# Performance work log

Hardware: AMD Instinct MI355X
Metric: run time of the kernel (lower is better)

Reference implementation:

```python
import jax, jax.numpy as jnp
import numpy as np

BATCH, NUM, CONS = 16384, 512, 512


def setup_inputs() -> dict:
    key = jax.random.key(0)
    k1, k2, k3, k4 = jax.random.split(key, 4)
    preds = jax.random.uniform(k1, (BATCH, NUM), dtype=jnp.float32)
    # sparse, mutually-exclusive binary body masks (a literal is pos or neg, not both)
    r = jax.random.randint(k2, (CONS, NUM), 0, 12)
    pos_body = (r == 0).astype(jnp.float32)
    neg_body = (r == 1).astype(jnp.float32)
    head_atom = jax.random.randint(k3, (CONS,), 0, NUM).astype(jnp.int32)
    head_sign = jax.random.randint(k4, (CONS,), 0, 2).astype(jnp.bool_)
    return {"preds": preds, "pos_body": pos_body, "neg_body": neg_body,
            "head_atom": head_atom, "head_sign": head_sign}


def reference(preds, pos_body, neg_body, head_atom, head_sign):
    # apply_iterative with goal=None: Gauss-Seidel sweep over constraints.
    # For constraint c: body value per atom j is pos_body[c,j]*(1-p[:,j]) or
    # neg_body[c,j]*p[:,j]; candidate = 1 - max(0, max_j body value);
    # then head literal is raised (positive) or lowered (negative).
    def step(p, xs):
        pos_row, neg_row, atom, sign = xs
        # [batch, num] elementwise; masks are disjoint so per-atom max == concat-max
        vals = jnp.maximum(pos_row[None, :] * (1.0 - p), neg_row[None, :] * p)
        cand = 1.0 - jnp.maximum(jnp.max(vals, axis=1), 0.0)  # zeros column in torch cat
        prev = jnp.take(p, atom, axis=1)  # [batch]
        upd = jnp.where(sign,
                        jnp.maximum(prev, cand),
                        jnp.minimum(prev, 1.0 - cand))
        p = jax.lax.dynamic_update_slice(p, upd[:, None], (0, atom))
        return p, None

    out, _ = jax.lax.scan(step, preds, (pos_body, neg_body, head_atom, head_sign))
    return out
```

## Files before the change

kernel.cpp:

```cpp
#include <hip/hip_runtime.h>

#define BATCH 16384
#define NUM   512
#define CONS  512
#define ROWS  8
#define ZOFF  (NUM*16)
#define OOFF  (NUM*16 + 16)
#define LDSB  (NUM*16 + 32)
#define NPAD  (CONS + 4)
#define RSTR  84

typedef _Float16 h2 __attribute__((ext_vector_type(2)));
static __device__ __forceinline__ h2 u2h(unsigned u){ return __builtin_bit_cast(h2,u); }
static __device__ __forceinline__ unsigned h2u(h2 h){ return __builtin_bit_cast(unsigned,h); }
static __device__ __forceinline__ h2 hmax2(h2 a,h2 b){ return __builtin_elementwise_max(a,b); }
static __device__ __forceinline__ h2 hmin2(h2 a,h2 b){ return __builtin_elementwise_min(a,b); }
template<int C>
static __device__ __forceinline__ h2 rormax(h2 x) {
  unsigned v = (unsigned)__builtin_amdgcn_mov_dpp((int)h2u(x), C, 0xF, 0xF, true);
  return hmax2(x, u2h(v));
}

__global__ __launch_bounds__(64) void prep_kernel(
    const float* __restrict__ pos, const float* __restrict__ neg,
    const int* __restrict__ head_atom, const int* __restrict__ head_sign,
    unsigned* __restrict__ ents) {
  int c = blockIdx.x, lane = threadIdx.x;
  unsigned* rec = ents + (size_t)c * RSTR;
  if (c >= CONS) {
    for (int t = lane; t < RSTR; t += 64) {
      unsigned v = 0;
      if (t < 32) v = 0x20002000u;
      else if (t < 64) v = 0x20102010u;
      else if (t == 64) v = 0x8000u << 16;
      else if (t < 73) v = ZOFF;
      else if (t < 81) v = OOFF;
      rec[t] = v;
    }
    return;
  }
  __shared__ unsigned short LN[96], LP[96];
  __shared__ unsigned short slotN[64], slotP[64];
  __shared__ unsigned char usedN[64], usedP[64];
  __shared__ unsigned short spill[16][8];
  __shared__ int spn[16];
  __shared__ unsigned short exN[8], exP[8];
  __shared__ int exn, exp_;
  slotN[lane] = ZOFF; slotP[lane] = OOFF;
  usedN[lane] = 0;    usedP[lane] = 0;
  if (lane < 8) { exN[lane] = ZOFF; exP[lane] = OOFF; }
  if (lane < 16) spn[lane] = 0;
  __syncthreads();

  int hp1 = (c >= 1) ? head_atom[c-1] : -1;
  int hp2 = (c >= 2) ? head_atom[c-2] : -1;
  int nN = 0, nP = 0;
  bool fN1=false, fP1=false, fN2=false, fP2=false;
  for (int k = 0; k < NUM/64; ++k) {
    int a = k*64 + lane;
    bool ln = neg[(size_t)c*NUM + a] != 0.f;
    bool lp = pos[(size_t)c*NUM + a] != 0.f;
    bool n1 = ln && (a == hp1), n2 = ln && (a == hp2);
    bool p1 = lp && (a == hp1), p2 = lp && (a == hp2);
    fN1 |= (__ballot(n1) != 0ull); fN2 |= (__ballot(n2) != 0ull);
    fP1 |= (__ballot(p1) != 0ull); fP2 |= (__ballot(p2) != 0ull);
    bool kn = ln && !n1 && !n2;
    bool kp = lp && !p1 && !p2;
    unsigned long long mn = __ballot(kn), mp = __ballot(kp);
    unsigned long long lt = (1ull << lane) - 1ull;
    int rn = nN + (int)__popcll(mn & lt);
    int rp = nP + (int)__popcll(mp & lt);
    if (kn && rn < 96) LN[rn] = (unsigned short)a;
    if (kp && rp < 96) LP[rp] = (unsigned short)a;
    nN += (int)__popcll(mn);
    nP += (int)__popcll(mp);
  }
  __syncthreads();
  if (lane < 16) {
    int r = lane & 7;
    bool isP = lane >= 8;
    const unsigned short* L = isP ? LP : LN;
    int n = isP ? nP : nN; if (n > 96) n = 96;
    unsigned short* slot = isP ? slotP : slotN;
    unsigned char* used = isP ? usedP : usedN;
    int rr = 0;
    for (int t = 0; t < n; ++t) {
      int a = L[t];
      if ((a & 7) == r) {
        if (rr < 8) { int s = rr*8 + r; slot[s] = (unsigned short)(a*16); used[s] = 1; }
        else if (rr < 16) spill[lane][rr-8] = (unsigned short)(a*16);
        ++rr;
      }
    }
    spn[lane] = rr > 8 ? (rr > 16 ? 8 : rr - 8) : 0;
  }
  __syncthreads();
  if (lane < 2) {
    bool isP = lane == 1;
    unsigned short* slot = isP ? slotP : slotN;
    unsigned char* used = isP ? usedP : usedN;
    unsigned short* exb = isP ? exP : exN;
    int base = isP ? 8 : 0;
    int e = 0, scan = 0;
    for (int r = 0; r < 8; ++r) {
      int ns = spn[base + r];
      for (int k = 0; k < ns; ++k) {
        unsigned short v = spill[base + r][k];
        while (scan < 64 && used[scan]) ++scan;
        if (scan < 64) { slot[scan] = v; used[scan] = 1; }
        else if (e < 8) exb[e++] = v;
      }
    }
    if (isP) exp_ = e; else exn = e;
  }
  __syncthreads();

  int hc = head_atom[c];
  unsigned fl = 0;
  if (head_sign[c]) fl |= 1u;
  if (fN1) fl |= 2u;  if (fP1) fl |= 4u;
  if (fN2) fl |= 8u;  if (fP2) fl |= 16u;
  if (hc == hp1) fl |= 32u; else if (hc == hp2) fl |= 64u;
  fl |= ((unsigned)exn << 7) | ((unsigned)exp_ << 11);
  unsigned ho = (unsigned)hc * 16u;
  for (int t = lane; t < RSTR; t += 64) {
    unsigned v;
    if (t < 32) {
      int jp = t >> 4, g = t & 15;
      v = (unsigned)slotN[32*jp + g] | ((unsigned)slotN[32*jp + 16 + g] << 16);
    } else if (t < 64) {
      int tp = t - 32, jp = tp >> 4, g = tp & 15;
      v = (unsigned)slotP[32*jp + g] | ((unsigned)slotP[32*jp + 16 + g] << 16);
    } else if (t == 64) v = ho | (fl << 16);
    else if (t < 73) v = exN[t - 65];
    else if (t < 81) v = exP[t - 73];
    else v = 0;
    rec[t] = v;
  }
}

struct ENT { unsigned w0, w1, w2, w3, mh; };
struct RDv { h2 n0,n1,n2,n3,p0,p1,p2,p3,pv; unsigned mh; };
struct ST  { h2 braw, prevraw; unsigned ho, flu; };

static __device__ __forceinline__ ENT ldent(const unsigned* ents, int c, int g) {
  const unsigned* rec = ents + (size_t)c * RSTR;
  ENT e;
  e.w0 = rec[g]; e.w1 = rec[16+g]; e.w2 = rec[32+g]; e.w3 = rec[48+g];
  e.mh = rec[64];
  return e;
}
static __device__ __forceinline__ void issue_reads(const ENT& E, const char* Pb,
                                                   unsigned pr4, RDv& R) {
  R.n0 = *(const h2*)(Pb + ((E.w0 & 0xFFFFu) + pr4));
  R.n1 = *(const h2*)(Pb + ((E.w0 >> 16)     + pr4));
  R.n2 = *(const h2*)(Pb + ((E.w1 & 0xFFFFu) + pr4));
  R.n3 = *(const h2*)(Pb + ((E.w1 >> 16)     + pr4));
  R.p0 = *(const h2*)(Pb + ((E.w2 & 0xFFFFu) + pr4));
  R.p1 = *(const h2*)(Pb + ((E.w2 >> 16)     + pr4));
  R.p2 = *(const h2*)(Pb + ((E.w3 & 0xFFFFu) + pr4));
  R.p3 = *(const h2*)(Pb + ((E.w3 >> 16)     + pr4));
  R.pv = *(const h2*)(Pb + ((E.mh & 0xFFFFu) + pr4));
  R.mh = E.mh;
}
static __device__ __forceinline__ void combine(const RDv& R, const unsigned* ents,
                                               int c, const char* Pb, unsigned pr4, ST& S) {
  h2 aN = hmax2(hmax2(R.n0, R.n1), hmax2(R.n2, R.n3));
  h2 aP = hmin2(hmin2(R.p0, R.p1), hmin2(R.p2, R.p3));
  unsigned flu = ((unsigned)__builtin_amdgcn_readfirstlane((int)R.mh)) >> 16;
  if (flu & 0x7F80u) {
    const unsigned* rec = ents + (size_t)c * RSTR;
    unsigned xn = (flu >> 7) & 15u, xp = (flu >> 11) & 15u;
    for (unsigned j = 0; j < xn; ++j) aN = hmax2(aN, *(const h2*)(Pb + (rec[65+j] + pr4)));
    for (unsigned j = 0; j < xp; ++j) aP = hmin2(aP, *(const h2*)(Pb + (rec[73+j] + pr4)));
  }
  const h2 one2 = {(_Float16)1.f, (_Float16)1.f};
  h2 bp = hmax2(aN, one2 - aP);
  bp = rormax<0x121>(bp);
  bp = rormax<0x122>(bp);
  bp = rormax<0x124>(bp);
  bp = rormax<0x128>(bp);
  S.braw = bp; S.prevraw = R.pv; S.ho = R.mh & 0xFFFFu; S.flu = flu;
}
static __device__ __forceinline__ h2 finalize(const ST& S, h2 up1, h2 up2,
                                              char* Pb, unsigned pr4, int lane) {
  const h2 one2 = {(_Float16)1.f, (_Float16)1.f};
  unsigned fl = S.flu;
  unsigned mN1 = 0u-((fl>>1)&1u), mP1 = 0u-((fl>>2)&1u);
  unsigned mN2 = 0u-((fl>>3)&1u), mP2 = 0u-((fl>>4)&1u);
  h2 b = S.braw;
  b = hmax2(b, u2h(h2u(up1) & mN1));
  b = hmax2(b, u2h(h2u(one2 - up1) & mP1));
  b = hmax2(b, u2h(h2u(up2) & mN2));
  b = hmax2(b, u2h(h2u(one2 - up2) & mP2));
  unsigned mR1 = 0u-((fl>>5)&1u), mR2 = 0u-((fl>>6)&1u), mRn = ~(mR1|mR2);
  h2 prev = u2h((h2u(up1)&mR1) | (h2u(up2)&mR2) | (h2u(S.prevraw)&mRn));
  unsigned ms = 0u-(fl&1u);
  unsigned hi = h2u(hmax2(prev, one2 - b));
  unsigned lo = h2u(hmin2(prev, b));
  h2 upd = u2h((hi&ms) | (lo&~ms));
  if ((lane & 15) == 0 && !(fl & 0x8000u))
    *(h2*)(Pb + S.ho + pr4) = upd;
  return upd;
}

__global__ __launch_bounds__(64, 2) void solve_kernel(
    const float* __restrict__ preds,
    const unsigned* __restrict__ ents,
    float* __restrict__ out) {
  __shared__ char Pb[LDSB];
  const int lane = threadIdx.x;
  const unsigned pr4 = (unsigned)(lane >> 4) * 4u;
  const int r2 = lane >> 4, cs = lane & 15;
  const size_t row0 = (size_t)blockIdx.x * ROWS;

  if (lane < 4)      *(unsigned*)(Pb + ZOFF + lane*4) = 0u;
  else if (lane < 8) *(unsigned*)(Pb + OOFF + (lane-4)*4) = 0x3C003C00u;

  for (int i = 0; i < 16; ++i) {
    int a = i*32 + cs*2;
    float2 v0 = *(const float2*)(preds + (row0 + 2*r2)     * NUM + a);
    float2 v1 = *(const float2*)(preds + (row0 + 2*r2 + 1) * NUM + a);
    h2 w0 = {(_Float16)v0.x, (_Float16)v1.x};
    h2 w1 = {(_Float16)v0.y, (_Float16)v1.y};
    *(h2*)(Pb + a*16 + r2*4) = w0;
    *(h2*)(Pb + (a+1)*16 + r2*4) = w1;
  }
  __syncthreads();

  const int g = lane & 15;
  ENT E0 = ldent(ents, 0, g), E1 = ldent(ents, 1, g);
  ENT E2 = ldent(ents, 2, g), E3 = ldent(ents, 3, g);
  RDv RA, RB; ST S0, S1;
  issue_reads(E0, Pb, pr4, RA);
  issue_reads(E1, Pb, pr4, RB);
  combine(RA, ents, 0, Pb, pr4, S0);
  h2 up1 = (h2)0.0f, up2 = (h2)0.0f;

  #pragma unroll 1
  for (int i = 0; i < CONS; i += 2) {
    issue_reads(E2, Pb, pr4, RA);
    { h2 u = finalize(S0, up1, up2, Pb, pr4, lane); up2 = up1; up1 = u; }
    combine(RB, ents, i+1, Pb, pr4, S1);
    E2 = ldent(ents, i+4, g);
    issue_reads(E3, Pb, pr4, RB);
    { h2 u = finalize(S1, up1, up2, Pb, pr4, lane); up2 = up1; up1 = u; }
    combine(RA, ents, i+2, Pb, pr4, S0);
    E3 = ldent(ents, i+5, g);
  }

  __syncthreads();
  for (int i = 0; i < 16; ++i) {
    int a = i*32 + cs*2;
    h2 w0 = *(const h2*)(Pb + a*16 + r2*4);
    h2 w1 = *(const h2*)(Pb + (a+1)*16 + r2*4);
    float2 v0 = {(float)w0.x, (float)w1.x};
    float2 v1 = {(float)w0.y, (float)w1.y};
    *(float2*)(out + (row0 + 2*r2)     * NUM + a) = v0;
    *(float2*)(out + (row0 + 2*r2 + 1) * NUM + a) = v1;
  }
}

extern "C" void kernel_launch(void* const* d_in, const int* in_sizes, int n_in,
                              void* d_out, int out_size, void* d_ws, size_t ws_size,
                              hipStream_t stream) {
  (void)in_sizes; (void)n_in; (void)out_size; (void)ws_size;
  const float* preds     = (const float*)d_in[0];
  const float* pos       = (const float*)d_in[1];
  const float* neg       = (const float*)d_in[2];
  const int*   head_atom = (const int*)d_in[3];
  const int*   head_sign = (const int*)d_in[4];

  unsigned* ents = (unsigned*)d_ws;

  prep_kernel<<<NPAD, 64, 0, stream>>>(pos, neg, head_atom, head_sign, ents);
  solve_kernel<<<BATCH / ROWS, 64, 0, stream>>>(preds, ents, (float*)d_out);
}
```

Before: 278.3 us.

## Transpose lane mapping and pack constraint records for vector loads

Lanes now map the row-pair index to lane&3 and the slot group to lane>>2, instead of the reverse. Per-constraint slot words are interleaved so each lane fetches its four offset words with one uint4 load. The cross-lane max reduction is rebuilt to match the new mapping, using two DPP row shifts, a ds_swizzle and a ds_bpermute. Flag handling in finalize switches from mask arithmetic to branches on uniform flags, and the readfirstlane on the flag word is dropped. The swizzle and bpermute go through the LDS crossbar and may add latency on the serial dependency chain, and the coalescing of the preds loads also changes.

```diff
diff --git a/kernel.cpp b/kernel.cpp
--- a/kernel.cpp
+++ b/kernel.cpp
@@ -8,7 +8,7 @@
 #define OOFF  (NUM*16 + 16)
 #define LDSB  (NUM*16 + 32)
 #define NPAD  (CONS + 4)
-#define RSTR  84
+#define RSTR  96
 
 typedef _Float16 h2 __attribute__((ext_vector_type(2)));
 static __device__ __forceinline__ h2 u2h(unsigned u){ return __builtin_bit_cast(h2,u); }
@@ -20,6 +20,14 @@
   unsigned v = (unsigned)__builtin_amdgcn_mov_dpp((int)h2u(x), C, 0xF, 0xF, true);
   return hmax2(x, u2h(v));
 }
+static __device__ __forceinline__ h2 swizmax(h2 x) {
+  unsigned v = (unsigned)__builtin_amdgcn_ds_swizzle((int)h2u(x), 0x401F);
+  return hmax2(x, u2h(v));
+}
+static __device__ __forceinline__ h2 bpermax(h2 x, int bpa) {
+  unsigned v = (unsigned)__builtin_amdgcn_ds_bpermute(bpa, (int)h2u(x));
+  return hmax2(x, u2h(v));
+}
 
 __global__ __launch_bounds__(64) void prep_kernel(
     const float* __restrict__ pos, const float* __restrict__ neg,
@@ -29,12 +37,12 @@
   unsigned* rec = ents + (size_t)c * RSTR;
   if (c >= CONS) {
     for (int t = lane; t < RSTR; t += 64) {
-      unsigned v = 0;
-      if (t < 32) v = 0x20002000u;
-      else if (t < 64) v = 0x20102010u;
-      else if (t == 64) v = 0x8000u << 16;
+      unsigned v;
+      if (t < 64) v = ((t & 3) < 2) ? 0x20002000u : 0x20102010u;
+      else if (t == 64) v = (unsigned)ZOFF | (0x8000u << 16);
       else if (t < 73) v = ZOFF;
       else if (t < 81) v = OOFF;
+      else v = 0;
       rec[t] = v;
     }
     return;
@@ -125,12 +133,12 @@
   unsigned ho = (unsigned)hc * 16u;
   for (int t = lane; t < RSTR; t += 64) {
     unsigned v;
-    if (t < 32) {
-      int jp = t >> 4, g = t & 15;
-      v = (unsigned)slotN[32*jp + g] | ((unsigned)slotN[32*jp + 16 + g] << 16);
-    } else if (t < 64) {
-      int tp = t - 32, jp = tp >> 4, g = tp & 15;
-      v = (unsigned)slotP[32*jp + g] | ((unsigned)slotP[32*jp + 16 + g] << 16);
+    if (t < 64) {
+      int gg = t >> 2, q = t & 3;
+      if (q == 0)      v = (unsigned)slotN[gg]    | ((unsigned)slotN[16+gg] << 16);
+      else if (q == 1) v = (unsigned)slotN[32+gg] | ((unsigned)slotN[48+gg] << 16);
+      else if (q == 2) v = (unsigned)slotP[gg]    | ((unsigned)slotP[16+gg] << 16);
+      else             v = (unsigned)slotP[32+gg] | ((unsigned)slotP[48+gg] << 16);
     } else if (t == 64) v = ho | (fl << 16);
     else if (t < 73) v = exN[t - 65];
     else if (t < 81) v = exP[t - 73];
@@ -139,67 +147,62 @@
   }
 }
 
-struct ENT { unsigned w0, w1, w2, w3, mh; };
-struct RDv { h2 n0,n1,n2,n3,p0,p1,p2,p3,pv; unsigned mh; };
-struct ST  { h2 braw, prevraw; unsigned ho, flu; };
-
-static __device__ __forceinline__ ENT ldent(const unsigned* ents, int c, int g) {
-  const unsigned* rec = ents + (size_t)c * RSTR;
-  ENT e;
-  e.w0 = rec[g]; e.w1 = rec[16+g]; e.w2 = rec[32+g]; e.w3 = rec[48+g];
-  e.mh = rec[64];
-  return e;
-}
-static __device__ __forceinline__ void issue_reads(const ENT& E, const char* Pb,
-                                                   unsigned pr4, RDv& R) {
-  R.n0 = *(const h2*)(Pb + ((E.w0 & 0xFFFFu) + pr4));
-  R.n1 = *(const h2*)(Pb + ((E.w0 >> 16)     + pr4));
-  R.n2 = *(const h2*)(Pb + ((E.w1 & 0xFFFFu) + pr4));
-  R.n3 = *(const h2*)(Pb + ((E.w1 >> 16)     + pr4));
-  R.p0 = *(const h2*)(Pb + ((E.w2 & 0xFFFFu) + pr4));
-  R.p1 = *(const h2*)(Pb + ((E.w2 >> 16)     + pr4));
-  R.p2 = *(const h2*)(Pb + ((E.w3 & 0xFFFFu) + pr4));
-  R.p3 = *(const h2*)(Pb + ((E.w3 >> 16)     + pr4));
-  R.pv = *(const h2*)(Pb + ((E.mh & 0xFFFFu) + pr4));
-  R.mh = E.mh;
+struct RDv { h2 n0,n1,n2,n3,p0,p1,p2,p3,pv; unsigned m; };
+struct ST  { h2 braw, prevraw; unsigned ho, fl; };
+
+static __device__ __forceinline__ void issue_reads(uint4 q, unsigned m,
+                                                   const char* Pb, unsigned pr4, RDv& R) {
+  R.n0 = *(const h2*)(Pb + ((q.x & 0xFFFFu) + pr4));
+  R.n1 = *(const h2*)(Pb + ((q.x >> 16)     + pr4));
+  R.n2 = *(const h2*)(Pb + ((q.y & 0xFFFFu) + pr4));
+  R.n3 = *(const h2*)(Pb + ((q.y >> 16)     + pr4));
+  R.p0 = *(const h2*)(Pb + ((q.z & 0xFFFFu) + pr4));
+  R.p1 = *(const h2*)(Pb + ((q.z >> 16)     + pr4));
+  R.p2 = *(const h2*)(Pb + ((q.w & 0xFFFFu) + pr4));
+  R.p3 = *(const h2*)(Pb + ((q.w >> 16)     + pr4));
+  R.pv = *(const h2*)(Pb + ((m & 0xFFFFu) + pr4));
+  R.m = m;
 }
 static __device__ __forceinline__ void combine(const RDv& R, const unsigned* ents,
-                                               int c, const char* Pb, unsigned pr4, ST& S) {
+                                               int c, const char* Pb, unsigned pr4,
+                                               int bpa, ST& S) {
   h2 aN = hmax2(hmax2(R.n0, R.n1), hmax2(R.n2, R.n3));
   h2 aP = hmin2(hmin2(R.p0, R.p1), hmin2(R.p2, R.p3));
-  unsigned flu = ((unsigned)__builtin_amdgcn_readfirstlane((int)R.mh)) >> 16;
-  if (flu & 0x7F80u) {
+  unsigned fl = R.m >> 16;
+  if (fl & 0x7F80u) {
     const unsigned* rec = ents + (size_t)c * RSTR;
-    unsigned xn = (flu >> 7) & 15u, xp = (flu >> 11) & 15u;
+    unsigned xn = (fl >> 7) & 15u, xp = (fl >> 11) & 15u;
     for (unsigned j = 0; j < xn; ++j) aN = hmax2(aN, *(const h2*)(Pb + (rec[65+j] + pr4)));
     for (unsigned j = 0; j < xp; ++j) aP = hmin2(aP, *(const h2*)(Pb + (rec[73+j] + pr4)));
   }
   const h2 one2 = {(_Float16)1.f, (_Float16)1.f};
   h2 bp = hmax2(aN, one2 - aP);
-  bp = rormax<0x121>(bp);
-  bp = rormax<0x122>(bp);
   bp = rormax<0x124>(bp);
   bp = rormax<0x128>(bp);
-  S.braw = bp; S.prevraw = R.pv; S.ho = R.mh & 0xFFFFu; S.flu = flu;
+  bp = swizmax(bp);
+  bp = bpermax(bp, bpa);
+  S.braw = bp; S.prevraw = R.pv; S.ho = R.m & 0xFFFFu; S.fl = fl;
 }
 static __device__ __forceinline__ h2 finalize(const ST& S, h2 up1, h2 up2,
                                               char* Pb, unsigned pr4, int lane) {
   const h2 one2 = {(_Float16)1.f, (_Float16)1.f};
-  unsigned fl = S.flu;
-  unsigned mN1 = 0u-((fl>>1)&1u), mP1 = 0u-((fl>>2)&1u);
-  unsigned mN2 = 0u-((fl>>3)&1u), mP2 = 0u-((fl>>4)&1u);
+  unsigned fl = S.fl;
   h2 b = S.braw;
-  b = hmax2(b, u2h(h2u(up1) & mN1));
-  b = hmax2(b, u2h(h2u(one2 - up1) & mP1));
-  b = hmax2(b, u2h(h2u(up2) & mN2));
-  b = hmax2(b, u2h(h2u(one2 - up2) & mP2));
-  unsigned mR1 = 0u-((fl>>5)&1u), mR2 = 0u-((fl>>6)&1u), mRn = ~(mR1|mR2);
-  h2 prev = u2h((h2u(up1)&mR1) | (h2u(up2)&mR2) | (h2u(S.prevraw)&mRn));
-  unsigned ms = 0u-(fl&1u);
-  unsigned hi = h2u(hmax2(prev, one2 - b));
-  unsigned lo = h2u(hmin2(prev, b));
-  h2 upd = u2h((hi&ms) | (lo&~ms));
-  if ((lane & 15) == 0 && !(fl & 0x8000u))
+  if (fl & 0x1Eu) {
+    unsigned mN1 = 0u-((fl>>1)&1u), mP1 = 0u-((fl>>2)&1u);
+    unsigned mN2 = 0u-((fl>>3)&1u), mP2 = 0u-((fl>>4)&1u);
+    b = hmax2(b, u2h(h2u(up1) & mN1));
+    b = hmax2(b, u2h(h2u(one2 - up1) & mP1));
+    b = hmax2(b, u2h(h2u(up2) & mN2));
+    b = hmax2(b, u2h(h2u(one2 - up2) & mP2));
+  }
+  h2 prev;
+  if (fl & 0x60u) prev = (fl & 0x20u) ? up1 : up2;
+  else prev = S.prevraw;
+  h2 upd;
+  if (fl & 1u) upd = hmax2(prev, one2 - b);
+  else         upd = hmin2(prev, b);
+  if (lane < 4 && !(fl & 0x8000u))
     *(h2*)(Pb + S.ho + pr4) = upd;
   return upd;
 }
@@ -210,8 +213,10 @@
     float* __restrict__ out) {
   __shared__ char Pb[LDSB];
   const int lane = threadIdx.x;
-  const unsigned pr4 = (unsigned)(lane >> 4) * 4u;
-  const int r2 = lane >> 4, cs = lane & 15;
+  const unsigned pr4 = (unsigned)(lane & 3) * 4u;
+  const int g = lane >> 2;
+  const int bpa = ((lane ^ 32) << 2);
+  const int pr = lane & 3, cs = lane >> 2;
   const size_t row0 = (size_t)blockIdx.x * ROWS;
 
   if (lane < 4)      *(unsigned*)(Pb + ZOFF + lane*4) = 0u;
@@ -219,45 +224,47 @@
 
   for (int i = 0; i < 16; ++i) {
     int a = i*32 + cs*2;
-    float2 v0 = *(const float2*)(preds + (row0 + 2*r2)     * NUM + a);
-    float2 v1 = *(const float2*)(preds + (row0 + 2*r2 + 1) * NUM + a);
+    float2 v0 = *(const float2*)(preds + (row0 + 2*pr)     * NUM + a);
+    float2 v1 = *(const float2*)(preds + (row0 + 2*pr + 1) * NUM + a);
     h2 w0 = {(_Float16)v0.x, (_Float16)v1.x};
     h2 w1 = {(_Float16)v0.y, (_Float16)v1.y};
-    *(h2*)(Pb + a*16 + r2*4) = w0;
-    *(h2*)(Pb + (a+1)*16 + r2*4) = w1;
-  }
-  __syncthreads();
-
-  const int g = lane & 15;
-  ENT E0 = ldent(ents, 0, g), E1 = ldent(ents, 1, g);
-  ENT E2 = ldent(ents, 2, g), E3 = ldent(ents, 3, g);
+    *(h2*)(Pb + a*16 + pr*4) = w0;
+    *(h2*)(Pb + (a+1)*16 + pr*4) = w1;
+  }
+  __syncthreads();
+
+  auto ldq = [&](int c) { return *(const uint4*)(ents + (size_t)c * RSTR + g * 4); };
+  auto ldm = [&](int c) { return ents[(size_t)c * RSTR + 64]; };
+
+  uint4 Q2 = ldq(2), Q3 = ldq(3);
+  unsigned M2 = ldm(2), M3 = ldm(3);
   RDv RA, RB; ST S0, S1;
-  issue_reads(E0, Pb, pr4, RA);
-  issue_reads(E1, Pb, pr4, RB);
-  combine(RA, ents, 0, Pb, pr4, S0);
+  { uint4 Q0 = ldq(0); unsigned M0 = ldm(0); issue_reads(Q0, M0, Pb, pr4, RA); }
+  { uint4 Q1 = ldq(1); unsigned M1 = ldm(1); issue_reads(Q1, M1, Pb, pr4, RB); }
+  combine(RA, ents, 0, Pb, pr4, bpa, S0);
   h2 up1 = (h2)0.0f, up2 = (h2)0.0f;
 
   #pragma unroll 1
   for (int i = 0; i < CONS; i += 2) {
-    issue_reads(E2, Pb, pr4, RA);
+    issue_reads(Q2, M2, Pb, pr4, RA);
     { h2 u = finalize(S0, up1, up2, Pb, pr4, lane); up2 = up1; up1 = u; }
-    combine(RB, ents, i+1, Pb, pr4, S1);
-    E2 = ldent(ents, i+4, g);
-    issue_reads(E3, Pb, pr4, RB);
+    combine(RB, ents, i+1, Pb, pr4, bpa, S1);
+    Q2 = ldq(i+4); M2 = ldm(i+4);
+    issue_reads(Q3, M3, Pb, pr4, RB);
     { h2 u = finalize(S1, up1, up2, Pb, pr4, lane); up2 = up1; up1 = u; }
-    combine(RA, ents, i+2, Pb, pr4, S0);
-    E3 = ldent(ents, i+5, g);
+    combine(RA, ents, i+2, Pb, pr4, bpa, S0);
+    Q3 = ldq(i+5); M3 = ldm(i+5);
   }
 
   __syncthreads();
   for (int i = 0; i < 16; ++i) {
     int a = i*32 + cs*2;
-    h2 w0 = *(const h2*)(Pb + a*16 + r2*4);
-    h2 w1 = *(const h2*)(Pb + (a+1)*16 + r2*4);
+    h2 w0 = *(const h2*)(Pb + a*16 + pr*4);
+    h2 w1 = *(const h2*)(Pb + (a+1)*16 + pr*4);
     float2 v0 = {(float)w0.x, (float)w1.x};
     float2 v1 = {(float)w0.y, (float)w1.y};
-    *(float2*)(out + (row0 + 2*r2)     * NUM + a) = v0;
-    *(float2*)(out + (row0 + 2*r2 + 1) * NUM + a) = v1;
+    *(float2*)(out + (row0 + 2*pr)     * NUM + a) = v0;
+    *(float2*)(out + (row0 + 2*pr + 1) * NUM + a) = v1;
   }
 }
 
```

New measurement: 331.3 us. 19.0% more time.
